# Kernel optimization log

Hardware: AMD Instinct MI355X
Metric: run time of the kernel (lower is better)

## Reference

```python
import jax, jax.numpy as jnp
import numpy as np

B, T, F, H, O = 16384, 128, 9, 128, 12


def setup_inputs() -> dict:
    key = jax.random.key(0)
    ks = jax.random.split(key, 14)
    s = 1.0 / np.sqrt(H)
    u = lambda k, shp: jax.random.uniform(k, shp, jnp.float32, -s, s)
    return {
        "x": jax.random.normal(ks[0], (B, T, F), jnp.float32),
        "W_in": u(ks[1], (H, F)), "b_in": u(ks[2], (H,)),
        "Wih0": u(ks[3], (4 * H, H)), "Whh0": u(ks[4], (4 * H, H)),
        "bih0": u(ks[5], (4 * H,)), "bhh0": u(ks[6], (4 * H,)),
        "Wih1": u(ks[7], (4 * H, H)), "Whh1": u(ks[8], (4 * H, H)),
        "bih1": u(ks[9], (4 * H,)), "bhh1": u(ks[10], (4 * H,)),
        "W_out": u(ks[11], (O, H)), "b_out": u(ks[12], (O,)),
    }


def _cell(h, c, xp, Wih, Whh, bih, bhh):
    # PyTorch LSTM gate order: i, f, g, o
    g = xp @ Wih.T + bih + h @ Whh.T + bhh  # [B, 4H]
    i, f, gg, o = jnp.split(g, 4, axis=-1)
    c = jax.nn.sigmoid(f) * c + jax.nn.sigmoid(i) * jnp.tanh(gg)
    h = jax.nn.sigmoid(o) * jnp.tanh(c)
    return h, c


def reference(x, W_in, b_in, Wih0, Whh0, bih0, bhh0, Wih1, Whh1, bih1, bhh1, W_out, b_out):
    # input projection, all timesteps at once: [B, T, H] -> scan over time
    xp = jnp.einsum('btf,hf->tbh', x, W_in) + b_in
    b = x.shape[0]
    zeros = jnp.zeros((b, H), x.dtype)
    carry0 = (zeros, zeros, zeros, zeros)  # h0, c0, h1, c1

    def step(carry, xt):
        h0, c0, h1, c1 = carry
        h0, c0 = _cell(h0, c0, xt, Wih0, Whh0, bih0, bhh0)
        h1, c1 = _cell(h1, c1, h0, Wih1, Whh1, bih1, bhh1)
        return (h0, c0, h1, c1), None

    (h0, c0, h1, c1), _ = jax.lax.scan(step, carry0, xp)
    # torch forward returns only the LAST step's output: out(h1) with softmax over dim=1
    return jax.nn.softmax(h1 @ W_out.T + b_out, axis=1)
```

## Files before the change

kernel.cpp:

```cpp
#include <hip/hip_runtime.h>
#include <hip/hip_bf16.h>
#include <stdint.h>
#include <stddef.h>

#define T_STEPS 128
#define F_IN 9
#define HID 128
#define OUT_N 12
#define XROW (T_STEPS * F_IN)
#define BATCH 16384

typedef __attribute__((ext_vector_type(8))) short bf16x8;
typedef __attribute__((ext_vector_type(4))) float f32x4;

#define MFMA16(a, b, c) __builtin_amdgcn_mfma_f32_16x16x32_bf16((a), (b), (c), 0, 0, 0)

__device__ __forceinline__ short f2bf(float f) {
  union { float f; uint32_t u; } v; v.f = f;
  return (short)((v.u + 0x7fffu + ((v.u >> 16) & 1u)) >> 16);
}
__device__ __forceinline__ short f2bf_hw(float f) {
  __hip_bfloat16 h = __float2bfloat16(f);
  union { __hip_bfloat16 h; short s; } u; u.h = h;
  return u.s;
}
__device__ __forceinline__ float frcp(float x) { return __builtin_amdgcn_rcpf(x); }
__device__ __forceinline__ float fexp2(float x) { return __builtin_amdgcn_exp2f(x); }
__device__ __forceinline__ float tanh_f(float x) {
  return 1.0f - 2.0f * frcp(1.0f + fexp2(2.8853900817779268f * x));
}

__global__ void prep_x(const float* __restrict__ x, short* __restrict__ xbf) {
  int idx = blockIdx.x * blockDim.x + threadIdx.x;
  int row = idx & (BATCH - 1), t = idx >> 14;
  const float* xp = x + (size_t)row * XROW + t * F_IN;
  short v[16];
#pragma unroll
  for (int j = 0; j < F_IN; ++j) v[j] = f2bf(xp[j]);
#pragma unroll
  for (int j = F_IN; j < 16; ++j) v[j] = 0;
  int4* dst = (int4*)(xbf + (size_t)idx * 16);
  dst[0] = ((const int4*)v)[0];
  dst[1] = ((const int4*)v)[1];
}

__global__ void prep_w0x(const float* __restrict__ W_in, const float* __restrict__ b_in,
                         const float* __restrict__ Wih0, const float* __restrict__ bih0,
                         const float* __restrict__ bhh0, const float* __restrict__ bih1,
                         const float* __restrict__ bhh1,
                         short* __restrict__ w0xf, float* __restrict__ b0x, float* __restrict__ b1) {
  int tid = threadIdx.x;
  int nt = tid >> 4, hl = tid & 15;
  int w = nt >> 2, g = nt & 3;
  int n = g * 128 + w * 16 + hl;
  float wacc[F_IN];
#pragma unroll
  for (int f = 0; f < F_IN; ++f) wacc[f] = 0.f;
  float bacc = 0.f;
  for (int h = 0; h < HID; ++h) {
    float wv = Wih0[n * HID + h];
    bacc += wv * b_in[h];
#pragma unroll
    for (int f = 0; f < F_IN; ++f) wacc[f] += wv * W_in[h * F_IN + f];
  }
  b0x[n] = bacc + bih0[n] + bhh0[n];
  b1[n] = bih1[n] + bhh1[n];
#pragma unroll
  for (int k = 0; k < 32; ++k) {
    int quad = k >> 3, j = k & 7;
    w0xf[((w * 4 + g) * 64 + quad * 16 + hl) * 8 + j] = (k < F_IN) ? f2bf(wacc[k]) : (short)0;
  }
}

__global__ void prep_wrec(const float* __restrict__ Whh0, const float* __restrict__ Wih1,
                          const float* __restrict__ Whh1,
                          short* __restrict__ whh0f, short* __restrict__ w1f) {
  int gt = blockIdx.x * blockDim.x + threadIdx.x;
  if (gt < 2048) {
    int kt = gt >> 9, rr = gt & 511;
    int nt = rr >> 4, hl = rr & 15;
    int w = nt >> 2, g = nt & 3;
    int n = g * 128 + w * 16 + hl;
#pragma unroll
    for (int k = 0; k < 32; ++k) {
      int quad = k >> 3, j = k & 7;
      whh0f[((w * 16 + kt * 4 + g) * 64 + quad * 16 + hl) * 8 + j] =
          f2bf(Whh0[n * HID + kt * 32 + k]);
    }
  } else {
    int g2 = gt - 2048;
    int kt = g2 >> 9, rr = g2 & 511;
    int nt = rr >> 4, hl = rr & 15;
    int w = nt >> 2, g = nt & 3;
    int n = g * 128 + w * 16 + hl;
#pragma unroll
    for (int k = 0; k < 32; ++k) {
      int quad = k >> 3, j = k & 7;
      int kg = kt * 32 + k;
      float v = (kg < HID) ? Wih1[n * HID + kg] : Whh1[n * HID + kg - HID];
      w1f[((w * 32 + kt * 4 + g) * 64 + quad * 16 + hl) * 8 + j] = f2bf(v);
    }
  }
}

__device__ __forceinline__ void lstm_step(
    int t, const short* __restrict__ xpl, const short* __restrict__ wp0,
    const short* __restrict__ wph, const short* __restrict__ wp1,
    const float* sb0, const float* sb1, float* c0buf, float* c1buf,
    const short* h0r, short* h0w, const short* h1r, short* h1w,
    int tid, int lane, int wr_off, int quad) {
  const f32x4 z4 = {0.f, 0.f, 0.f, 0.f};
  const short* xt = xpl + (size_t)t * 262144;

  f32x4 acc1[4][4];
  {
    const short* wb = wp1;
    bf16x8 b0_ = *(const bf16x8*)(wb);
    bf16x8 b1_ = *(const bf16x8*)(wb + 512);
    bf16x8 b2_ = *(const bf16x8*)(wb + 1024);
    bf16x8 b3_ = *(const bf16x8*)(wb + 1536);
#pragma unroll
    for (int mt = 0; mt < 4; ++mt) {
      bf16x8 af = *(const bf16x8*)(h0r + ((mt * 4 + 0) * 64 + lane) * 8);
      acc1[mt][0] = MFMA16(af, b0_, z4);
      acc1[mt][1] = MFMA16(af, b1_, z4);
      acc1[mt][2] = MFMA16(af, b2_, z4);
      acc1[mt][3] = MFMA16(af, b3_, z4);
    }
  }
#pragma clang loop unroll_count(3)
  for (int kt = 1; kt < 4; ++kt) {
    const short* wb = wp1 + kt * 2048;
    bf16x8 b0_ = *(const bf16x8*)(wb);
    bf16x8 b1_ = *(const bf16x8*)(wb + 512);
    bf16x8 b2_ = *(const bf16x8*)(wb + 1024);
    bf16x8 b3_ = *(const bf16x8*)(wb + 1536);
#pragma unroll
    for (int mt = 0; mt < 4; ++mt) {
      bf16x8 af = *(const bf16x8*)(h0r + ((mt * 4 + kt) * 64 + lane) * 8);
      acc1[mt][0] = MFMA16(af, b0_, acc1[mt][0]);
      acc1[mt][1] = MFMA16(af, b1_, acc1[mt][1]);
      acc1[mt][2] = MFMA16(af, b2_, acc1[mt][2]);
      acc1[mt][3] = MFMA16(af, b3_, acc1[mt][3]);
    }
  }
#pragma clang loop unroll_count(2)
  for (int kt = 0; kt < 4; ++kt) {
    const short* wb = wp1 + (kt + 4) * 2048;
    bf16x8 b0_ = *(const bf16x8*)(wb);
    bf16x8 b1_ = *(const bf16x8*)(wb + 512);
    bf16x8 b2_ = *(const bf16x8*)(wb + 1024);
    bf16x8 b3_ = *(const bf16x8*)(wb + 1536);
#pragma unroll
    for (int mt = 0; mt < 4; ++mt) {
      bf16x8 af = *(const bf16x8*)(h1r + ((mt * 4 + kt) * 64 + lane) * 8);
      acc1[mt][0] = MFMA16(af, b0_, acc1[mt][0]);
      acc1[mt][1] = MFMA16(af, b1_, acc1[mt][1]);
      acc1[mt][2] = MFMA16(af, b2_, acc1[mt][2]);
      acc1[mt][3] = MFMA16(af, b3_, acc1[mt][3]);
    }
  }
#pragma unroll
  for (int mt = 0; mt < 4; ++mt) {
    f32x4 cp = *(const f32x4*)(c1buf + 4 * (mt * 512 + tid));
    f32x4 cn;
#pragma unroll
    for (int r = 0; r < 4; ++r) {
      float gi = frcp(1.0f + fexp2(fmaf(-1.4426950408889634f, acc1[mt][0][r], sb1[0])));
      float gf = frcp(1.0f + fexp2(fmaf(-1.4426950408889634f, acc1[mt][1][r], sb1[1])));
      float gg = 1.0f - 2.0f * frcp(1.0f + fexp2(fmaf(2.8853900817779268f, acc1[mt][2][r], sb1[2])));
      float go = frcp(1.0f + fexp2(fmaf(-1.4426950408889634f, acc1[mt][3][r], sb1[3])));
      cn[r] = gf * cp[r] + gi * gg;
      float hn = go * tanh_f(cn[r]);
      h1w[mt * 2048 + r * 8 + wr_off] = f2bf_hw(hn);
    }
    *(f32x4*)(c1buf + 4 * (mt * 512 + tid)) = cn;
  }
  f32x4 acc0[4][4];
  {
    bf16x8 b0_ = *(const bf16x8*)(wp0);
    bf16x8 b1_ = *(const bf16x8*)(wp0 + 512);
    bf16x8 b2_ = *(const bf16x8*)(wp0 + 1024);
    bf16x8 b3_ = *(const bf16x8*)(wp0 + 1536);
#pragma unroll
    for (int mt = 0; mt < 4; ++mt) {
      bf16x8 xf = {0, 0, 0, 0, 0, 0, 0, 0};
      if (quad < 2) xf = *(const bf16x8*)(xt + mt * 256);
      acc0[mt][0] = MFMA16(xf, b0_, z4);
      acc0[mt][1] = MFMA16(xf, b1_, z4);
      acc0[mt][2] = MFMA16(xf, b2_, z4);
      acc0[mt][3] = MFMA16(xf, b3_, z4);
    }
  }
#pragma clang loop unroll_count(2)
  for (int kt = 0; kt < 4; ++kt) {
    const short* wb = wph + kt * 2048;
    bf16x8 b0_ = *(const bf16x8*)(wb);
    bf16x8 b1_ = *(const bf16x8*)(wb + 512);
    bf16x8 b2_ = *(const bf16x8*)(wb + 1024);
    bf16x8 b3_ = *(const bf16x8*)(wb + 1536);
#pragma unroll
    for (int mt = 0; mt < 4; ++mt) {
      bf16x8 af = *(const bf16x8*)(h0r + ((mt * 4 + kt) * 64 + lane) * 8);
      acc0[mt][0] = MFMA16(af, b0_, acc0[mt][0]);
      acc0[mt][1] = MFMA16(af, b1_, acc0[mt][1]);
      acc0[mt][2] = MFMA16(af, b2_, acc0[mt][2]);
      acc0[mt][3] = MFMA16(af, b3_, acc0[mt][3]);
    }
  }
#pragma unroll
  for (int mt = 0; mt < 4; ++mt) {
    f32x4 cp = *(const f32x4*)(c0buf + 4 * (mt * 512 + tid));
    f32x4 cn;
#pragma unroll
    for (int r = 0; r < 4; ++r) {
      float gi = frcp(1.0f + fexp2(fmaf(-1.4426950408889634f, acc0[mt][0][r], sb0[0])));
      float gf = frcp(1.0f + fexp2(fmaf(-1.4426950408889634f, acc0[mt][1][r], sb0[1])));
      float gg = 1.0f - 2.0f * frcp(1.0f + fexp2(fmaf(2.8853900817779268f, acc0[mt][2][r], sb0[2])));
      float go = frcp(1.0f + fexp2(fmaf(-1.4426950408889634f, acc0[mt][3][r], sb0[3])));
      cn[r] = gf * cp[r] + gi * gg;
      float hn = go * tanh_f(cn[r]);
      h0w[mt * 2048 + r * 8 + wr_off] = f2bf_hw(hn);
    }
    *(f32x4*)(c0buf + 4 * (mt * 512 + tid)) = cn;
  }
  __syncthreads();
}

__global__ void __launch_bounds__(512)
lstm_main(const short* __restrict__ xbf, const short* __restrict__ w0xf,
          const short* __restrict__ whh0f, const short* __restrict__ w1f,
          const float* __restrict__ b0x, const float* __restrict__ b1,
          const float* __restrict__ Wout, const float* __restrict__ bout,
          float* __restrict__ out) {
  __shared__ short h0a[8192], h0b[8192], h1a[8192], h1b[8192];
  __shared__ float h1fp_c0[64 * HID];
  __shared__ float c1buf[64 * HID];
  __shared__ float lg[64 * OUT_N];

  const int tid = threadIdx.x;
  const int w = tid >> 6, lane = tid & 63;
  const int quad = lane >> 4, c = lane & 15;
  const int rowbase = blockIdx.x * 64;

  {
    for (int i = tid; i < 4096; i += 512) {
      ((int*)h0a)[i] = 0; ((int*)h0b)[i] = 0; ((int*)h1a)[i] = 0; ((int*)h1b)[i] = 0;
    }
    for (int i = tid; i < 8192; i += 512) { h1fp_c0[i] = 0.f; c1buf[i] = 0.f; }
  }

  const short* wp0 = w0xf + (w * 4) * 512 + lane * 8;
  const short* wph = whh0f + (w * 16) * 512 + lane * 8;
  const short* wp1 = w1f + (w * 32) * 512 + lane * 8;

  const short* xpl = xbf + ((size_t)(rowbase + c) << 4) + ((quad & 1) << 3);

  float sb0[4], sb1[4];
#pragma unroll
  for (int g = 0; g < 4; ++g) {
    int n = g * 128 + w * 16 + c;
    float bv0 = b0x[n], bv1 = b1[n];
    sb0[g] = (g == 2) ? 2.8853900817779268f * bv0 : -1.4426950408889634f * bv0;
    sb1[g] = (g == 2) ? 2.8853900817779268f * bv1 : -1.4426950408889634f * bv1;
  }

  const int kt_w = w >> 1;
  const int klocal = ((w & 1) << 4) + c;
  const int quadA = klocal >> 3;
  const int jA = klocal & 7;
  const int wr_off = (kt_w * 64 + quadA * 16 + quad * 4) * 8 + jA;

  const f32x4 z4 = {0.f, 0.f, 0.f, 0.f};

  __syncthreads();

  {
    f32x4 acc[4][4];
    {
      bf16x8 b0_ = *(const bf16x8*)(wp0);
      bf16x8 b1_ = *(const bf16x8*)(wp0 + 512);
      bf16x8 b2_ = *(const bf16x8*)(wp0 + 1024);
      bf16x8 b3_ = *(const bf16x8*)(wp0 + 1536);
#pragma unroll
      for (int mt = 0; mt < 4; ++mt) {
        bf16x8 xf = {0, 0, 0, 0, 0, 0, 0, 0};
        if (quad < 2) xf = *(const bf16x8*)(xpl + mt * 256);
        acc[mt][0] = MFMA16(xf, b0_, z4);
        acc[mt][1] = MFMA16(xf, b1_, z4);
        acc[mt][2] = MFMA16(xf, b2_, z4);
        acc[mt][3] = MFMA16(xf, b3_, z4);
      }
    }
#pragma unroll
    for (int mt = 0; mt < 4; ++mt) {
      f32x4 cn;
#pragma unroll
      for (int r = 0; r < 4; ++r) {
        float gi = frcp(1.0f + fexp2(fmaf(-1.4426950408889634f, acc[mt][0][r], sb0[0])));
        float gg = 1.0f - 2.0f * frcp(1.0f + fexp2(fmaf(2.8853900817779268f, acc[mt][2][r], sb0[2])));
        float go = frcp(1.0f + fexp2(fmaf(-1.4426950408889634f, acc[mt][3][r], sb0[3])));
        cn[r] = gi * gg;
        float hn = go * tanh_f(cn[r]);
        h0a[mt * 2048 + r * 8 + wr_off] = f2bf_hw(hn);
      }
      *(f32x4*)(h1fp_c0 + 4 * (mt * 512 + tid)) = cn;
    }
  }
  __syncthreads();

#pragma clang loop unroll(disable)
  for (int t = 1; t < 127; t += 2) {
    lstm_step(t,     xpl, wp0, wph, wp1, sb0, sb1, h1fp_c0, c1buf, h0a, h0b, h1a, h1b,
              tid, lane, wr_off, quad);
    lstm_step(t + 1, xpl, wp0, wph, wp1, sb0, sb1, h1fp_c0, c1buf, h0b, h0a, h1b, h1a,
              tid, lane, wr_off, quad);
  }
  lstm_step(127, xpl, wp0, wph, wp1, sb0, sb1, h1fp_c0, c1buf, h0a, h0b, h1a, h1b,
            tid, lane, wr_off, quad);

  {
    f32x4 acc[4][4];
    {
      const short* wb = wp1;
      bf16x8 b0_ = *(const bf16x8*)(wb);
      bf16x8 b1_ = *(const bf16x8*)(wb + 512);
      bf16x8 b2_ = *(const bf16x8*)(wb + 1024);
      bf16x8 b3_ = *(const bf16x8*)(wb + 1536);
#pragma unroll
      for (int mt = 0; mt < 4; ++mt) {
        bf16x8 af = *(const bf16x8*)(h0b + ((mt * 4 + 0) * 64 + lane) * 8);
        acc[mt][0] = MFMA16(af, b0_, z4);
        acc[mt][1] = MFMA16(af, b1_, z4);
        acc[mt][2] = MFMA16(af, b2_, z4);
        acc[mt][3] = MFMA16(af, b3_, z4);
      }
    }
#pragma unroll
    for (int kt = 1; kt < 4; ++kt) {
      const short* wb = wp1 + kt * 2048;
      bf16x8 b0_ = *(const bf16x8*)(wb);
      bf16x8 b1_ = *(const bf16x8*)(wb + 512);
      bf16x8 b2_ = *(const bf16x8*)(wb + 1024);
      bf16x8 b3_ = *(const bf16x8*)(wb + 1536);
#pragma unroll
      for (int mt = 0; mt < 4; ++mt) {
        bf16x8 af = *(const bf16x8*)(h0b + ((mt * 4 + kt) * 64 + lane) * 8);
        acc[mt][0] = MFMA16(af, b0_, acc[mt][0]);
        acc[mt][1] = MFMA16(af, b1_, acc[mt][1]);
        acc[mt][2] = MFMA16(af, b2_, acc[mt][2]);
        acc[mt][3] = MFMA16(af, b3_, acc[mt][3]);
      }
    }
#pragma unroll
    for (int kt = 0; kt < 4; ++kt) {
      const short* wb = wp1 + (kt + 4) * 2048;
      bf16x8 b0_ = *(const bf16x8*)(wb);
      bf16x8 b1_ = *(const bf16x8*)(wb + 512);
      bf16x8 b2_ = *(const bf16x8*)(wb + 1024);
      bf16x8 b3_ = *(const bf16x8*)(wb + 1536);
#pragma unroll
      for (int mt = 0; mt < 4; ++mt) {
        bf16x8 af = *(const bf16x8*)(h1b + ((mt * 4 + kt) * 64 + lane) * 8);
        acc[mt][0] = MFMA16(af, b0_, acc[mt][0]);
        acc[mt][1] = MFMA16(af, b1_, acc[mt][1]);
        acc[mt][2] = MFMA16(af, b2_, acc[mt][2]);
        acc[mt][3] = MFMA16(af, b3_, acc[mt][3]);
      }
    }
    __syncthreads();
#pragma unroll
    for (int mt = 0; mt < 4; ++mt) {
      f32x4 cp = *(const f32x4*)(c1buf + 4 * (mt * 512 + tid));
#pragma unroll
      for (int r = 0; r < 4; ++r) {
        float gi = frcp(1.0f + fexp2(fmaf(-1.4426950408889634f, acc[mt][0][r], sb1[0])));
        float gf = frcp(1.0f + fexp2(fmaf(-1.4426950408889634f, acc[mt][1][r], sb1[1])));
        float gg = 1.0f - 2.0f * frcp(1.0f + fexp2(fmaf(2.8853900817779268f, acc[mt][2][r], sb1[2])));
        float go = frcp(1.0f + fexp2(fmaf(-1.4426950408889634f, acc[mt][3][r], sb1[3])));
        float cn = gf * cp[r] + gi * gg;
        float hn = go * tanh_f(cn);
        h1fp_c0[(mt * 16 + quad * 4 + r) * HID + w * 16 + c] = hn;
      }
    }
  }
  __syncthreads();

  {
    int row = tid >> 3, og = tid & 7;
    for (int oc = og; oc < OUT_N; oc += 8) {
      float s = bout[oc];
      const float* wo = Wout + oc * HID;
      const float* hr = h1fp_c0 + row * HID;
#pragma unroll 8
      for (int k = 0; k < HID; ++k) s += hr[k] * wo[k];
      lg[row * OUT_N + oc] = s;
    }
  }
  __syncthreads();
  if (tid < 64) {
    int row = tid;
    float m = lg[row * OUT_N];
#pragma unroll
    for (int oc = 1; oc < OUT_N; ++oc) m = fmaxf(m, lg[row * OUT_N + oc]);
    float e[OUT_N];
    float s = 0.f;
#pragma unroll
    for (int oc = 0; oc < OUT_N; ++oc) {
      e[oc] = __expf(lg[row * OUT_N + oc] - m);
      s += e[oc];
    }
    float inv = 1.0f / s;
    float* orow = out + (size_t)(rowbase + row) * OUT_N;
#pragma unroll
    for (int oc = 0; oc < OUT_N; ++oc) orow[oc] = e[oc] * inv;
  }
}

extern "C" void kernel_launch(void* const* d_in, const int* in_sizes, int n_in,
                              void* d_out, int out_size, void* d_ws, size_t ws_size,
                              hipStream_t stream) {
  const float* x    = (const float*)d_in[0];
  const float* W_in = (const float*)d_in[1];
  const float* b_in = (const float*)d_in[2];
  const float* Wih0 = (const float*)d_in[3];
  const float* Whh0 = (const float*)d_in[4];
  const float* bih0 = (const float*)d_in[5];
  const float* bhh0 = (const float*)d_in[6];
  const float* Wih1 = (const float*)d_in[7];
  const float* Whh1 = (const float*)d_in[8];
  const float* bih1 = (const float*)d_in[9];
  const float* bhh1 = (const float*)d_in[10];
  const float* Wout = (const float*)d_in[11];
  const float* bout = (const float*)d_in[12];
  float* out = (float*)d_out;

  short* w0xf  = (short*)d_ws;
  short* whh0f = w0xf + 16384;
  short* w1f   = whh0f + 65536;
  float* b0x   = (float*)(w1f + 131072);
  float* b1    = b0x + 512;
  short* xbf   = (short*)(b1 + 512);

  prep_x<<<(BATCH * T_STEPS) / 256, 256, 0, stream>>>(x, xbf);
  prep_w0x<<<1, 512, 0, stream>>>(W_in, b_in, Wih0, bih0, bhh0, bih1, bhh1, w0xf, b0x, b1);
  prep_wrec<<<12, 512, 0, stream>>>(Whh0, Wih1, Whh1, whh0f, w1f);
  lstm_main<<<256, 512, 0, stream>>>(xbf, w0xf, whh0f, w1f, b0x, b1, Wout, bout, out);
}
```

Baseline: 1.184 ms.

## Alternate layer-phase order across waves to overlap MFMA and transcendental work

Adds a second step variant that computes layer 0 before layer 1, and assigns half the waves (chosen by a wave-index parity pattern) to it while the other half keep the layer-1-then-layer-0 order. The intent is that, within one SIMD, one wave's matrix-core phase lines up with another wave's exponential/activation phase, so MFMA and VALU work overlap instead of all waves contending for the same unit at once. Both variants read h0r in their layer-1 MFMAs, so the new order should give the same result as the original, since layer 1 at step t uses the previous h0. The cost is a duplicated step body, which enlarges the code and may raise register pressure, and divergent control flow between waves.

```diff
diff --git a/kernel.cpp b/kernel.cpp
--- a/kernel.cpp
+++ b/kernel.cpp
@@ -103,7 +103,8 @@
   }
 }
 
-__device__ __forceinline__ void lstm_step(
+
+__device__ __forceinline__ void lstm_step_p1p0(
     int t, const short* __restrict__ xpl, const short* __restrict__ wp0,
     const short* __restrict__ wph, const short* __restrict__ wp1,
     const float* sb0, const float* sb1, float* c0buf, float* c1buf,
@@ -223,6 +224,149 @@
       h0w[mt * 2048 + r * 8 + wr_off] = f2bf_hw(hn);
     }
     *(f32x4*)(c0buf + 4 * (mt * 512 + tid)) = cn;
+  }
+  __syncthreads();
+}
+
+__device__ __forceinline__ void lstm_step_p0p1(
+    int t, const short* __restrict__ xpl, const short* __restrict__ wp0,
+    const short* __restrict__ wph, const short* __restrict__ wp1,
+    const float* sb0, const float* sb1, float* c0buf, float* c1buf,
+    const short* h0r, short* h0w, const short* h1r, short* h1w,
+    int tid, int lane, int wr_off, int quad) {
+  const f32x4 z4 = {0.f, 0.f, 0.f, 0.f};
+  const short* xt = xpl + (size_t)t * 262144;
+  bf16x8 xf[4];
+#pragma unroll
+  for (int mt = 0; mt < 4; ++mt) {
+    bf16x8 v = {0, 0, 0, 0, 0, 0, 0, 0};
+    if (quad < 2) v = *(const bf16x8*)(xt + mt * 256);
+    xf[mt] = v;
+  }
+  f32x4 acc0[4][4];
+  {
+    const short* wb = wph;
+    bf16x8 b0_ = *(const bf16x8*)(wb);
+    bf16x8 b1_ = *(const bf16x8*)(wb + 512);
+    bf16x8 b2_ = *(const bf16x8*)(wb + 1024);
+    bf16x8 b3_ = *(const bf16x8*)(wb + 1536);
+#pragma unroll
+    for (int mt = 0; mt < 4; ++mt) {
+      bf16x8 af = *(const bf16x8*)(h0r + ((mt * 4 + 0) * 64 + lane) * 8);
+      acc0[mt][0] = MFMA16(af, b0_, z4);
+      acc0[mt][1] = MFMA16(af, b1_, z4);
+      acc0[mt][2] = MFMA16(af, b2_, z4);
+      acc0[mt][3] = MFMA16(af, b3_, z4);
+    }
+  }
+#pragma clang loop unroll_count(3)
+  for (int kt = 1; kt < 4; ++kt) {
+    const short* wb = wph + kt * 2048;
+    bf16x8 b0_ = *(const bf16x8*)(wb);
+    bf16x8 b1_ = *(const bf16x8*)(wb + 512);
+    bf16x8 b2_ = *(const bf16x8*)(wb + 1024);
+    bf16x8 b3_ = *(const bf16x8*)(wb + 1536);
+#pragma unroll
+    for (int mt = 0; mt < 4; ++mt) {
+      bf16x8 af = *(const bf16x8*)(h0r + ((mt * 4 + kt) * 64 + lane) * 8);
+      acc0[mt][0] = MFMA16(af, b0_, acc0[mt][0]);
+      acc0[mt][1] = MFMA16(af, b1_, acc0[mt][1]);
+      acc0[mt][2] = MFMA16(af, b2_, acc0[mt][2]);
+      acc0[mt][3] = MFMA16(af, b3_, acc0[mt][3]);
+    }
+  }
+  {
+    bf16x8 b0_ = *(const bf16x8*)(wp0);
+    bf16x8 b1_ = *(const bf16x8*)(wp0 + 512);
+    bf16x8 b2_ = *(const bf16x8*)(wp0 + 1024);
+    bf16x8 b3_ = *(const bf16x8*)(wp0 + 1536);
+#pragma unroll
+    for (int mt = 0; mt < 4; ++mt) {
+      acc0[mt][0] = MFMA16(xf[mt], b0_, acc0[mt][0]);
+      acc0[mt][1] = MFMA16(xf[mt], b1_, acc0[mt][1]);
+      acc0[mt][2] = MFMA16(xf[mt], b2_, acc0[mt][2]);
+      acc0[mt][3] = MFMA16(xf[mt], b3_, acc0[mt][3]);
+    }
+  }
+#pragma unroll
+  for (int mt = 0; mt < 4; ++mt) {
+    f32x4 cp = *(const f32x4*)(c0buf + 4 * (mt * 512 + tid));
+    f32x4 cn;
+#pragma unroll
+    for (int r = 0; r < 4; ++r) {
+      float gi = frcp(1.0f + fexp2(fmaf(-1.4426950408889634f, acc0[mt][0][r], sb0[0])));
+      float gf = frcp(1.0f + fexp2(fmaf(-1.4426950408889634f, acc0[mt][1][r], sb0[1])));
+      float gg = 1.0f - 2.0f * frcp(1.0f + fexp2(fmaf(2.8853900817779268f, acc0[mt][2][r], sb0[2])));
+      float go = frcp(1.0f + fexp2(fmaf(-1.4426950408889634f, acc0[mt][3][r], sb0[3])));
+      cn[r] = gf * cp[r] + gi * gg;
+      float hn = go * tanh_f(cn[r]);
+      h0w[mt * 2048 + r * 8 + wr_off] = f2bf_hw(hn);
+    }
+    *(f32x4*)(c0buf + 4 * (mt * 512 + tid)) = cn;
+  }
+  f32x4 acc1[4][4];
+  {
+    const short* wb = wp1;
+    bf16x8 b0_ = *(const bf16x8*)(wb);
+    bf16x8 b1_ = *(const bf16x8*)(wb + 512);
+    bf16x8 b2_ = *(const bf16x8*)(wb + 1024);
+    bf16x8 b3_ = *(const bf16x8*)(wb + 1536);
+#pragma unroll
+    for (int mt = 0; mt < 4; ++mt) {
+      bf16x8 af = *(const bf16x8*)(h0r + ((mt * 4 + 0) * 64 + lane) * 8);
+      acc1[mt][0] = MFMA16(af, b0_, z4);
+      acc1[mt][1] = MFMA16(af, b1_, z4);
+      acc1[mt][2] = MFMA16(af, b2_, z4);
+      acc1[mt][3] = MFMA16(af, b3_, z4);
+    }
+  }
+#pragma clang loop unroll_count(3)
+  for (int kt = 1; kt < 4; ++kt) {
+    const short* wb = wp1 + kt * 2048;
+    bf16x8 b0_ = *(const bf16x8*)(wb);
+    bf16x8 b1_ = *(const bf16x8*)(wb + 512);
+    bf16x8 b2_ = *(const bf16x8*)(wb + 1024);
+    bf16x8 b3_ = *(const bf16x8*)(wb + 1536);
+#pragma unroll
+    for (int mt = 0; mt < 4; ++mt) {
+      bf16x8 af = *(const bf16x8*)(h0r + ((mt * 4 + kt) * 64 + lane) * 8);
+      acc1[mt][0] = MFMA16(af, b0_, acc1[mt][0]);
+      acc1[mt][1] = MFMA16(af, b1_, acc1[mt][1]);
+      acc1[mt][2] = MFMA16(af, b2_, acc1[mt][2]);
+      acc1[mt][3] = MFMA16(af, b3_, acc1[mt][3]);
+    }
+  }
+#pragma clang loop unroll_count(2)
+  for (int kt = 0; kt < 4; ++kt) {
+    const short* wb = wp1 + (kt + 4) * 2048;
+    bf16x8 b0_ = *(const bf16x8*)(wb);
+    bf16x8 b1_ = *(const bf16x8*)(wb + 512);
+    bf16x8 b2_ = *(const bf16x8*)(wb + 1024);
+    bf16x8 b3_ = *(const bf16x8*)(wb + 1536);
+#pragma unroll
+    for (int mt = 0; mt < 4; ++mt) {
+      bf16x8 af = *(const bf16x8*)(h1r + ((mt * 4 + kt) * 64 + lane) * 8);
+      acc1[mt][0] = MFMA16(af, b0_, acc1[mt][0]);
+      acc1[mt][1] = MFMA16(af, b1_, acc1[mt][1]);
+      acc1[mt][2] = MFMA16(af, b2_, acc1[mt][2]);
+      acc1[mt][3] = MFMA16(af, b3_, acc1[mt][3]);
+    }
+  }
+#pragma unroll
+  for (int mt = 0; mt < 4; ++mt) {
+    f32x4 cp = *(const f32x4*)(c1buf + 4 * (mt * 512 + tid));
+    f32x4 cn;
+#pragma unroll
+    for (int r = 0; r < 4; ++r) {
+      float gi = frcp(1.0f + fexp2(fmaf(-1.4426950408889634f, acc1[mt][0][r], sb1[0])));
+      float gf = frcp(1.0f + fexp2(fmaf(-1.4426950408889634f, acc1[mt][1][r], sb1[1])));
+      float gg = 1.0f - 2.0f * frcp(1.0f + fexp2(fmaf(2.8853900817779268f, acc1[mt][2][r], sb1[2])));
+      float go = frcp(1.0f + fexp2(fmaf(-1.4426950408889634f, acc1[mt][3][r], sb1[3])));
+      cn[r] = gf * cp[r] + gi * gg;
+      float hn = go * tanh_f(cn[r]);
+      h1w[mt * 2048 + r * 8 + wr_off] = f2bf_hw(hn);
+    }
+    *(f32x4*)(c1buf + 4 * (mt * 512 + tid)) = cn;
   }
   __syncthreads();
 }
@@ -309,15 +453,27 @@
   }
   __syncthreads();
 
+  if (((w ^ (w >> 2)) & 1) == 0) {
 #pragma clang loop unroll(disable)
-  for (int t = 1; t < 127; t += 2) {
-    lstm_step(t,     xpl, wp0, wph, wp1, sb0, sb1, h1fp_c0, c1buf, h0a, h0b, h1a, h1b,
-              tid, lane, wr_off, quad);
-    lstm_step(t + 1, xpl, wp0, wph, wp1, sb0, sb1, h1fp_c0, c1buf, h0b, h0a, h1b, h1a,
-              tid, lane, wr_off, quad);
-  }
-  lstm_step(127, xpl, wp0, wph, wp1, sb0, sb1, h1fp_c0, c1buf, h0a, h0b, h1a, h1b,
-            tid, lane, wr_off, quad);
+    for (int t = 1; t < 127; t += 2) {
+      lstm_step_p1p0(t,     xpl, wp0, wph, wp1, sb0, sb1, h1fp_c0, c1buf, h0a, h0b, h1a, h1b,
+                     tid, lane, wr_off, quad);
+      lstm_step_p1p0(t + 1, xpl, wp0, wph, wp1, sb0, sb1, h1fp_c0, c1buf, h0b, h0a, h1b, h1a,
+                     tid, lane, wr_off, quad);
+    }
+    lstm_step_p1p0(127, xpl, wp0, wph, wp1, sb0, sb1, h1fp_c0, c1buf, h0a, h0b, h1a, h1b,
+                   tid, lane, wr_off, quad);
+  } else {
+#pragma clang loop unroll(disable)
+    for (int t = 1; t < 127; t += 2) {
+      lstm_step_p0p1(t,     xpl, wp0, wph, wp1, sb0, sb1, h1fp_c0, c1buf, h0a, h0b, h1a, h1b,
+                     tid, lane, wr_off, quad);
+      lstm_step_p0p1(t + 1, xpl, wp0, wph, wp1, sb0, sb1, h1fp_c0, c1buf, h0b, h0a, h1b, h1a,
+                     tid, lane, wr_off, quad);
+    }
+    lstm_step_p0p1(127, xpl, wp0, wph, wp1, sb0, sb1, h1fp_c0, c1buf, h0a, h0b, h1a, h1b,
+                   tid, lane, wr_off, quad);
+  }
 
   {
     f32x4 acc[4][4];
```

Result: slower. 1.486 ms (+25.6%).
